# Performance work log

Measured on AMD Instinct MI355X. Metric: run time of the kernel, lower is better.

## Reference

```python
import jax, jax.numpy as jnp
import numpy as np

N_LIC, N_EMP, N_CON = 40000, 80000, 60000
D_LIC, D_EMP, D_CON = 256, 128, 192
H = 256
E_P, E_Q = 1280000, 640000


def setup_inputs() -> dict:
    key = jax.random.key(0)
    ks = jax.random.split(key, 13)
    s = 0.05
    return {
        "x_lic": jax.random.normal(ks[0], (N_LIC, D_LIC), jnp.float32),
        "x_emp": jax.random.normal(ks[1], (N_EMP, D_EMP), jnp.float32),
        "x_con": jax.random.normal(ks[2], (N_CON, D_CON), jnp.float32),
        "Wl_p": jax.random.normal(ks[3], (D_EMP, H), jnp.float32) * s,
        "Wr_p": jax.random.normal(ks[4], (D_LIC, H), jnp.float32) * s,
        "b_p": jax.random.normal(ks[5], (H,), jnp.float32) * s,
        "Wl_q": jax.random.normal(ks[6], (D_CON, H), jnp.float32) * s,
        "Wr_q": jax.random.normal(ks[7], (D_LIC, H), jnp.float32) * s,
        "b_q": jax.random.normal(ks[8], (H,), jnp.float32) * s,
        "ei_p_src": jax.random.randint(ks[9], (E_P,), 0, N_EMP, jnp.int64),
        "ei_p_dst": jax.random.randint(ks[10], (E_P,), 0, N_LIC, jnp.int64),
        "ei_q_src": jax.random.randint(ks[11], (E_Q,), 0, N_CON, jnp.int64),
        "ei_q_dst": jax.random.randint(ks[12], (E_Q,), 0, N_LIC, jnp.int64),
    }


def _sage_conv(x_src, x_dst, src, dst, Wl, Wr, b):
    """PyG SAGEConv (mean aggr): lin_l(mean_neighbors) + lin_r(x_dst) + bias."""
    n_dst = x_dst.shape[0]
    # gather src features per edge, scatter-sum to dst nodes
    agg = jax.ops.segment_sum(x_src[src], dst, num_segments=n_dst)  # [n_dst, d_src]
    deg = jax.ops.segment_sum(jnp.ones(src.shape, x_src.dtype), dst, num_segments=n_dst)
    agg = agg / jnp.maximum(deg, 1.0)[:, None]  # zero-degree nodes -> 0 (PyG semantics)
    return agg @ Wl + x_dst @ Wr + b


def reference(x_lic, x_emp, x_con, Wl_p, Wr_p, b_p, Wl_q, Wr_q, b_q,
              ei_p_src, ei_p_dst, ei_q_src, ei_q_dst):
    # to_hetero dispatch: two relations target 'licitacion'; aggr='mean' across relations.
    out_p = _sage_conv(x_emp, x_lic, ei_p_src, ei_p_dst, Wl_p, Wr_p, b_p)  # empresa->licitacion
    out_q = _sage_conv(x_con, x_lic, ei_q_src, ei_q_dst, Wl_q, Wr_q, b_q)  # contrato->licitacion
    # forward returns x_dict['licitacion'] after relu; other dst types are dead code.
    return jax.nn.relu(0.5 * (out_p + out_q))
```

## Files before the change

kernel.cpp:

```cpp
#include <hip/hip_runtime.h>

#define N_LIC 40000
#define N_EMP 80000
#define N_CON 60000
#define D_EMP 128
#define D_CON 192
#define HDIM  256
#define E_P   1280000
#define E_Q   640000
#define E_T   (E_P + E_Q)

#define NSEG  64
#define SEGW  (2 * NSEG)
#define SUBR  (N_LIC / NSEG)
#define NBPRE ((E_T + 2047) / 2048)

#define OFF_AGGP   0
#define OFF_STG    OFF_AGGP
#define OFF_XE     (OFF_AGGP + 2560000)
#define OFF_AGGQ   OFF_XE
#define OFF_XC     (OFF_XE + 5120000)
#define OFF_BPK    (OFF_XC + 5760000)
#define OFF_BIAS   (OFF_BPK + 73728)
#define OFF_CNT    (OFF_BIAS + 256)
#define OFF_SEGT   (OFF_CNT + 2 * N_LIC)
#define OFF_SEGB   (OFF_SEGT + 128)
#define OFF_SEGC   (OFF_SEGB + 128)
#define OFF_OFFP   (OFF_SEGC + 128)
#define OFF_OFFQ   (OFF_OFFP + N_LIC)
#define OFF_SRTP   (OFF_OFFQ + N_LIC)
#define OFF_SRTQ   (OFF_SRTP + E_P)

typedef short bf16x8 __attribute__((ext_vector_type(8)));
typedef float f32x4 __attribute__((ext_vector_type(4)));

__device__ __forceinline__ ushort f2bf(float f) {
    union { float f; uint u; } v; v.f = f;
    return (ushort)((v.u + 0x7fffu + ((v.u >> 16) & 1u)) >> 16);
}

__device__ __forceinline__ void acc2(uint u, float& lo, float& hi) {
    union { uint u; float f; } a, b;
    a.u = u << 16;
    b.u = u & 0xffff0000u;
    lo += a.f; hi += b.f;
}

__device__ __forceinline__ uint packbf(float lo, float hi) {
    return (uint)f2bf(lo) | ((uint)f2bf(hi) << 16);
}

__global__ void prep_kernel(const float* __restrict__ Wlp, const float* __restrict__ Wlq,
                            const float* __restrict__ Wrp, const float* __restrict__ Wrq,
                            const float* __restrict__ bp, const float* __restrict__ bq,
                            ushort* __restrict__ Bpk, float* __restrict__ bias) {
    int tid = blockIdx.x * 256 + threadIdx.x;
    if (tid < 256 * 576) {
        int n = tid / 576, k = tid - n * 576;
        float v;
        if (k < 128)      v = Wlp[k * 256 + n];
        else if (k < 320) v = Wlq[(k - 128) * 256 + n];
        else              v = Wrp[(k - 320) * 256 + n] + Wrq[(k - 320) * 256 + n];
        Bpk[tid] = f2bf(v);
    } else if (tid < 256 * 576 + 256) {
        int j = tid - 256 * 576;
        bias[j] = bp[j] + bq[j];
    }
}

#define C_XE (N_EMP * 128 / 4)
#define C_XC (N_CON * 192 / 4)
__global__ __launch_bounds__(256) void conv_pre_kernel(
        const float* __restrict__ xemp, const float* __restrict__ xcon,
        ushort* __restrict__ xe, ushort* __restrict__ xc,
        const int* __restrict__ dp, const int* __restrict__ dq,
        int* __restrict__ segtot) {
    __shared__ int lc[SEGW];
    int b = blockIdx.x;
    int t = threadIdx.x;
    if (b < NBPRE) {
        if (t < SEGW) lc[t] = 0;
        __syncthreads();
        int base = b * 2048 + t;
        #pragma unroll
        for (int i = 0; i < 8; i++) {
            int e = base + i * 256;
            if (e < E_T) {
                int d, rel;
                if (e < E_P) { d = __builtin_nontemporal_load(&dp[e]); rel = 0; }
                else         { d = __builtin_nontemporal_load(&dq[e - E_P]); rel = 1; }
                atomicAdd(&lc[rel * NSEG + d / SUBR], 1);
            }
        }
        __syncthreads();
        if (t < SEGW && lc[t] > 0) atomicAdd(&segtot[t], lc[t]);
    } else {
        int tid = (b - NBPRE) * 256 + t;
        const float* src; ushort* dst; int i;
        if (tid < C_XE) { src = xemp; dst = xe; i = tid; }
        else            { src = xcon; dst = xc; i = tid - C_XE; }
        float4 v = ((const float4*)src)[i];
        uint2 o;
        o.x = packbf(v.x, v.y);
        o.y = packbf(v.z, v.w);
        ((uint2*)dst)[i] = o;
    }
}

__global__ void segbase_kernel(const int* __restrict__ segtot,
                               int* __restrict__ segbase, int* __restrict__ segcur) {
    if (threadIdx.x == 0) {
        int run = 0;
        for (int i = 0; i < SEGW; i++) {
            segbase[i] = run; segcur[i] = run;
            run += segtot[i];
        }
    }
}

__global__ __launch_bounds__(256) void partition_kernel(const int* __restrict__ sp,
                                                        const int* __restrict__ dp,
                                                        const int* __restrict__ sq,
                                                        const int* __restrict__ dq,
                                                        int* __restrict__ segcur,
                                                        uint* __restrict__ stg) {
    __shared__ int lc[SEGW], inc[SEGW], lb[SEGW], gb[SEGW];
    __shared__ uint srtd[2048];
    __shared__ uchar sid[2048];
    int t = threadIdx.x;
    if (t < SEGW) lc[t] = 0;
    __syncthreads();
    int seg[8], lo[8]; uint pk[8];
    int base = blockIdx.x * 2048 + t;
    #pragma unroll
    for (int i = 0; i < 8; i++) {
        int e = base + i * 256;
        seg[i] = -1;
        if (e < E_T) {
            int d, s, rel;
            if (e < E_P) {
                d = __builtin_nontemporal_load(&dp[e]);
                s = __builtin_nontemporal_load(&sp[e]); rel = 0;
            } else {
                int eq = e - E_P;
                d = __builtin_nontemporal_load(&dq[eq]);
                s = __builtin_nontemporal_load(&sq[eq]); rel = 1;
            }
            int sl = d / SUBR;
            int dl = d - sl * SUBR;
            seg[i] = rel * NSEG + sl;
            pk[i] = ((uint)dl << 17) | (uint)s;
            lo[i] = atomicAdd(&lc[seg[i]], 1);
        }
    }
    __syncthreads();
    if (t < SEGW) inc[t] = lc[t];
    __syncthreads();
    #pragma unroll
    for (int off = 1; off < SEGW; off <<= 1) {
        int v = (t >= off && t < SEGW) ? inc[t - off] : 0;
        __syncthreads();
        if (t < SEGW) inc[t] += v;
        __syncthreads();
    }
    if (t < SEGW) {
        lb[t] = inc[t] - lc[t];
        gb[t] = lc[t] > 0 ? atomicAdd(&segcur[t], lc[t]) : 0;
    }
    __syncthreads();
    #pragma unroll
    for (int i = 0; i < 8; i++) {
        if (seg[i] >= 0) {
            int p = lb[seg[i]] + lo[i];
            srtd[p] = pk[i];
            sid[p] = (uchar)seg[i];
        }
    }
    __syncthreads();
    int tot = inc[SEGW - 1];
    for (int p = t; p < tot; p += 256) {
        int s = sid[p];
        stg[gb[s] + (p - lb[s])] = srtd[p];
    }
}

#define LCAP 22528
__global__ __launch_bounds__(1024) void sort_kernel(const int* __restrict__ segbase,
                                                    const int* __restrict__ segcur,
                                                    const uint* __restrict__ stg,
                                                    int* __restrict__ srtp, int* __restrict__ srtq,
                                                    int* __restrict__ offp, int* __restrict__ offq,
                                                    int* __restrict__ cnt) {
    __shared__ int lcnt[SUBR], lcur[SUBR];
    __shared__ int sc[640];
    __shared__ uint buf[LCAP];
    int s = blockIdx.x;
    int rel = s >> 6;
    int beg = segbase[s], end = segcur[s];
    int t = threadIdx.x;
    if (t < SUBR) { lcnt[t] = 0; lcur[t] = 0; }
    __syncthreads();
    for (int idx = beg + t; idx < end; idx += 1024)
        atomicAdd(&lcnt[stg[idx] >> 17], 1);
    __syncthreads();
    if (t < 640) sc[t] = (t < SUBR) ? lcnt[t] : 0;
    __syncthreads();
    #pragma unroll
    for (int off = 1; off < 640; off <<= 1) {
        int v = (t >= off && t < 640) ? sc[t - off] : 0;
        __syncthreads();
        if (t < 640) sc[t] += v;
        __syncthreads();
    }
    int rb = (rel == 0) ? beg : beg - E_P;
    int* srt = (rel == 0) ? srtp : srtq;
    for (int idx = beg + t; idx < end; idx += 1024) {
        uint p = stg[idx];
        int dl = (int)(p >> 17);
        int pos = sc[dl] - lcnt[dl] + atomicAdd(&lcur[dl], 1);
        uint sv = p & 0x1FFFFu;
        if (pos < LCAP) buf[pos] = sv;
        else srt[rb + pos] = (int)sv;
    }
    __syncthreads();
    int n = end - beg;
    int m = n < LCAP ? n : LCAP;
    for (int p = t; p < m; p += 1024) srt[rb + p] = (int)buf[p];
    int dbase = (s & (NSEG - 1)) * SUBR;
    int* offs = (rel == 0) ? offp : offq;
    int* cn = (rel == 0) ? cnt : cnt + N_LIC;
    if (t < SUBR) {
        offs[dbase + t] = rb + sc[t] - lcnt[t];
        cn[dbase + t] = lcnt[t];
    }
}

__global__ __launch_bounds__(256) void aggP_kernel(const ushort* __restrict__ xe,
                                                   const int* __restrict__ offs,
                                                   const int* __restrict__ cnt,
                                                   const int* __restrict__ sorted,
                                                   ushort* __restrict__ agg) {
    int g = blockIdx.x * 16 + (threadIdx.x >> 4);
    int c = threadIdx.x & 15;
    int beg = offs[g], deg = cnt[g], end = beg + deg;
    float a0=0,a1=0,a2=0,a3=0,a4=0,a5=0,a6=0,a7=0;
    int eb = beg;
    for (; eb + 16 <= end; eb += 16) {
        int my = sorted[eb + c];
        #pragma unroll
        for (int j = 0; j < 16; j++) {
            int s = __shfl(my, j, 16);
            uint4 v = *(const uint4*)(xe + (size_t)s * D_EMP + c * 8);
            acc2(v.x, a0, a1); acc2(v.y, a2, a3);
            acc2(v.z, a4, a5); acc2(v.w, a6, a7);
        }
    }
    int n = end - eb;
    if (n > 0) {
        int my = (c < n) ? sorted[eb + c] : 0;
        for (int j = 0; j < n; j++) {
            int s = __shfl(my, j, 16);
            uint4 v = *(const uint4*)(xe + (size_t)s * D_EMP + c * 8);
            acc2(v.x, a0, a1); acc2(v.y, a2, a3);
            acc2(v.z, a4, a5); acc2(v.w, a6, a7);
        }
    }
    float inv = 1.0f / fmaxf((float)deg, 1.0f);
    uint4 o;
    o.x = packbf(a0 * inv, a1 * inv);
    o.y = packbf(a2 * inv, a3 * inv);
    o.z = packbf(a4 * inv, a5 * inv);
    o.w = packbf(a6 * inv, a7 * inv);
    *(uint4*)(agg + (size_t)g * D_EMP + c * 8) = o;
}

__global__ __launch_bounds__(256) void aggQ_kernel(const ushort* __restrict__ xc,
                                                   const int* __restrict__ offs,
                                                   const int* __restrict__ cnt,
                                                   const int* __restrict__ sorted,
                                                   ushort* __restrict__ agg) {
    int g = blockIdx.x * 16 + (threadIdx.x >> 4);
    int c = threadIdx.x & 15;
    int beg = offs[g], deg = cnt[g], end = beg + deg;
    float a0=0,a1=0,a2=0,a3=0,a4=0,a5=0,a6=0,a7=0,a8=0,a9=0,a10=0,a11=0;
    int eb = beg;
    for (; eb + 16 <= end; eb += 16) {
        int my = sorted[eb + c];
        #pragma unroll 8
        for (int j = 0; j < 16; j++) {
            int s = __shfl(my, j, 16);
            const ushort* row = xc + (size_t)s * D_CON + c * 12;
            uint2 v0 = *(const uint2*)(row + 0);
            uint2 v1 = *(const uint2*)(row + 4);
            uint2 v2 = *(const uint2*)(row + 8);
            acc2(v0.x, a0, a1);  acc2(v0.y, a2, a3);
            acc2(v1.x, a4, a5);  acc2(v1.y, a6, a7);
            acc2(v2.x, a8, a9);  acc2(v2.y, a10, a11);
        }
    }
    int n = end - eb;
    if (n > 0) {
        int my = (c < n) ? sorted[eb + c] : 0;
        for (int j = 0; j < n; j++) {
            int s = __shfl(my, j, 16);
            const ushort* row = xc + (size_t)s * D_CON + c * 12;
            uint2 v0 = *(const uint2*)(row + 0);
            uint2 v1 = *(const uint2*)(row + 4);
            uint2 v2 = *(const uint2*)(row + 8);
            acc2(v0.x, a0, a1);  acc2(v0.y, a2, a3);
            acc2(v1.x, a4, a5);  acc2(v1.y, a6, a7);
            acc2(v2.x, a8, a9);  acc2(v2.y, a10, a11);
        }
    }
    float inv = 1.0f / fmaxf((float)deg, 1.0f);
    ushort* o = agg + (size_t)g * D_CON + c * 12;
    uint2 w0, w1, w2;
    w0.x = packbf(a0 * inv, a1 * inv);   w0.y = packbf(a2 * inv, a3 * inv);
    w1.x = packbf(a4 * inv, a5 * inv);   w1.y = packbf(a6 * inv, a7 * inv);
    w2.x = packbf(a8 * inv, a9 * inv);   w2.y = packbf(a10 * inv, a11 * inv);
    *(uint2*)(o + 0) = w0;
    *(uint2*)(o + 4) = w1;
    *(uint2*)(o + 8) = w2;
}

__global__ __launch_bounds__(256) void gemm_kernel(
    const ushort* __restrict__ aggp, const ushort* __restrict__ aggq,
    const float* __restrict__ xlic, const ushort* __restrict__ Bpk,
    const float* __restrict__ bias, float* __restrict__ out)
{
    __shared__ __align__(16) ushort As[2][64 * 40];
    __shared__ __align__(16) ushort Bs[2][256 * 40];

    const int t = threadIdx.x;
    const int m0 = blockIdx.x * 64;
    const int lane = t & 63;
    const int wave = t >> 6;
    const int arow = t >> 2;
    const int achk = t & 3;
    const int l15 = lane & 15;
    const int lh  = lane >> 4;

    f32x4 acc[4][4];
    #pragma unroll
    for (int i = 0; i < 4; i++)
        #pragma unroll
        for (int j = 0; j < 4; j++)
            acc[i][j] = (f32x4){0.f, 0.f, 0.f, 0.f};

    uint4 pb0, pb1, pb2, pb3, pa0, pa1;

    #define REG_LOAD(k0)                                                                     \
    {                                                                                        \
        pb0 = *(const uint4*)(Bpk + (size_t)(arow +   0) * 576 + (k0) + achk * 8);           \
        pb1 = *(const uint4*)(Bpk + (size_t)(arow +  64) * 576 + (k0) + achk * 8);           \
        pb2 = *(const uint4*)(Bpk + (size_t)(arow + 128) * 576 + (k0) + achk * 8);           \
        pb3 = *(const uint4*)(Bpk + (size_t)(arow + 192) * 576 + (k0) + achk * 8);           \
        if ((k0) < 128) {                                                                    \
            pa0 = *(const uint4*)(aggp + (size_t)(m0 + arow) * 128 + (k0) + achk * 8);       \
        } else if ((k0) < 320) {                                                             \
            pa0 = *(const uint4*)(aggq + (size_t)(m0 + arow) * 192 + ((k0) - 128) + achk * 8); \
        } else {                                                                             \
            const float* src_ = xlic + (size_t)(m0 + arow) * 256 + ((k0) - 320) + achk * 8;  \
            pa0 = *(const uint4*)(src_ + 0);                                                 \
            pa1 = *(const uint4*)(src_ + 4);                                                 \
        }                                                                                    \
    }

    #define LDS_WRITE(b, k0)                                                                 \
    {                                                                                        \
        uint4 aw;                                                                            \
        if ((k0) < 320) aw = pa0;                                                            \
        else {                                                                               \
            union { uint4 u; float f[4]; } c0, c1;                                           \
            c0.u = pa0; c1.u = pa1;                                                          \
            aw.x = packbf(c0.f[0], c0.f[1]);                                                 \
            aw.y = packbf(c0.f[2], c0.f[3]);                                                 \
            aw.z = packbf(c1.f[0], c1.f[1]);                                                 \
            aw.w = packbf(c1.f[2], c1.f[3]);                                                 \
        }                                                                                    \
        *(uint4*)(&As[b][arow * 40 + achk * 8]) = aw;                                        \
        *(uint4*)(&Bs[b][(arow +   0) * 40 + achk * 8]) = pb0;                               \
        *(uint4*)(&Bs[b][(arow +  64) * 40 + achk * 8]) = pb1;                               \
        *(uint4*)(&Bs[b][(arow + 128) * 40 + achk * 8]) = pb2;                               \
        *(uint4*)(&Bs[b][(arow + 192) * 40 + achk * 8]) = pb3;                               \
    }

    #define COMPUTE(b)                                                                       \
    {                                                                                        \
        bf16x8 af[4], bfr[4];                                                                \
        _Pragma("unroll")                                                                    \
        for (int mt = 0; mt < 4; mt++)                                                       \
            af[mt] = *(const bf16x8*)(&As[b][(mt * 16 + l15) * 40 + lh * 8]);                \
        _Pragma("unroll")                                                                    \
        for (int nt = 0; nt < 4; nt++)                                                       \
            bfr[nt] = *(const bf16x8*)(&Bs[b][(wave * 64 + nt * 16 + l15) * 40 + lh * 8]);   \
        _Pragma("unroll")                                                                    \
        for (int mt = 0; mt < 4; mt++)                                                       \
            _Pragma("unroll")                                                                \
            for (int nt = 0; nt < 4; nt++)                                                   \
                acc[mt][nt] = __builtin_amdgcn_mfma_f32_16x16x32_bf16(af[mt], bfr[nt], acc[mt][nt], 0, 0, 0); \
    }

    REG_LOAD(0);
    LDS_WRITE(0, 0);
    __syncthreads();

    int cur = 0;
    for (int k0 = 32; k0 < 576; k0 += 32) {
        REG_LOAD(k0);
        COMPUTE(cur);
        LDS_WRITE(cur ^ 1, k0);
        __syncthreads();
        cur ^= 1;
    }
    COMPUTE(cur);

    #pragma unroll
    for (int nt = 0; nt < 4; nt++) {
        int n = wave * 64 + nt * 16 + l15;
        float bv = bias[n];
        #pragma unroll
        for (int mt = 0; mt < 4; mt++) {
            #pragma unroll
            for (int r = 0; r < 4; r++) {
                int m = m0 + mt * 16 + lh * 4 + r;
                float v = 0.5f * (acc[mt][nt][r] + bv);
                out[(size_t)m * 256 + n] = fmaxf(v, 0.f);
            }
        }
    }
    #undef REG_LOAD
    #undef LDS_WRITE
    #undef COMPUTE
}

extern "C" void kernel_launch(void* const* d_in, const int* in_sizes, int n_in,
                              void* d_out, int out_size, void* d_ws, size_t ws_size,
                              hipStream_t stream) {
    const float* x_lic = (const float*)d_in[0];
    const float* x_emp = (const float*)d_in[1];
    const float* x_con = (const float*)d_in[2];
    const float* Wl_p  = (const float*)d_in[3];
    const float* Wr_p  = (const float*)d_in[4];
    const float* b_p   = (const float*)d_in[5];
    const float* Wl_q  = (const float*)d_in[6];
    const float* Wr_q  = (const float*)d_in[7];
    const float* b_q   = (const float*)d_in[8];
    const int* ei_p_src = (const int*)d_in[9];
    const int* ei_p_dst = (const int*)d_in[10];
    const int* ei_q_src = (const int*)d_in[11];
    const int* ei_q_dst = (const int*)d_in[12];

    float* ws = (float*)d_ws;
    ushort* aggp = (ushort*)(ws + OFF_AGGP);
    ushort* aggq = (ushort*)(ws + OFF_AGGQ);
    uint*  stg  = (uint*)(ws + OFF_STG);
    ushort* xe   = (ushort*)(ws + OFF_XE);
    ushort* xc   = (ushort*)(ws + OFF_XC);
    ushort* Bpk  = (ushort*)(ws + OFF_BPK);
    float* bias  = ws + OFF_BIAS;
    int* cnt  = (int*)(ws + OFF_CNT);
    int* segt = (int*)(ws + OFF_SEGT);
    int* segb = (int*)(ws + OFF_SEGB);
    int* segc = (int*)(ws + OFF_SEGC);
    int* offp = (int*)(ws + OFF_OFFP);
    int* offq = (int*)(ws + OFF_OFFQ);
    int* srtp = (int*)(ws + OFF_SRTP);
    int* srtq = (int*)(ws + OFF_SRTQ);
    float* out = (float*)d_out;

    hipMemsetAsync(segt, 0, SEGW * sizeof(int), stream);

    prep_kernel<<<(256 * 576 + 256 + 255) / 256, 256, 0, stream>>>(Wl_p, Wl_q, Wr_p, Wr_q, b_p, b_q, Bpk, bias);

    conv_pre_kernel<<<NBPRE + (C_XE + C_XC) / 256, 256, 0, stream>>>(
        x_emp, x_con, xe, xc, ei_p_dst, ei_q_dst, segt);

    segbase_kernel<<<1, 64, 0, stream>>>(segt, segb, segc);
    partition_kernel<<<NBPRE, 256, 0, stream>>>(ei_p_src, ei_p_dst, ei_q_src, ei_q_dst, segc, stg);

    sort_kernel<<<SEGW, 1024, 0, stream>>>(segb, segc, stg, srtp, srtq, offp, offq, cnt);

    aggP_kernel<<<N_LIC / 16, 256, 0, stream>>>(xe, offp, cnt, srtp, aggp);
    aggQ_kernel<<<N_LIC / 16, 256, 0, stream>>>(xc, offq, cnt + N_LIC, srtq, aggq);

    gemm_kernel<<<N_LIC / 64, 256, 0, stream>>>(aggp, aggq, x_lic, Bpk, bias, out);
}
```

Before: 354.6 us.

## Fuse neighbor aggregation for both relations into the GEMM kernel

```diff
diff --git a/kernel.cpp b/kernel.cpp
--- a/kernel.cpp
+++ b/kernel.cpp
@@ -18,7 +18,6 @@
 #define OFF_AGGP   0
 #define OFF_STG    OFF_AGGP
 #define OFF_XE     (OFF_AGGP + 2560000)
-#define OFF_AGGQ   OFF_XE
 #define OFF_XC     (OFF_XE + 5120000)
 #define OFF_BPK    (OFF_XC + 5760000)
 #define OFF_BIAS   (OFF_BPK + 73728)
@@ -235,104 +234,105 @@
     }
 }
 
-__global__ __launch_bounds__(256) void aggP_kernel(const ushort* __restrict__ xe,
-                                                   const int* __restrict__ offs,
-                                                   const int* __restrict__ cnt,
-                                                   const int* __restrict__ sorted,
-                                                   ushort* __restrict__ agg) {
-    int g = blockIdx.x * 16 + (threadIdx.x >> 4);
-    int c = threadIdx.x & 15;
-    int beg = offs[g], deg = cnt[g], end = beg + deg;
-    float a0=0,a1=0,a2=0,a3=0,a4=0,a5=0,a6=0,a7=0;
-    int eb = beg;
-    for (; eb + 16 <= end; eb += 16) {
-        int my = sorted[eb + c];
-        #pragma unroll
-        for (int j = 0; j < 16; j++) {
-            int s = __shfl(my, j, 16);
-            uint4 v = *(const uint4*)(xe + (size_t)s * D_EMP + c * 8);
-            acc2(v.x, a0, a1); acc2(v.y, a2, a3);
-            acc2(v.z, a4, a5); acc2(v.w, a6, a7);
-        }
-    }
-    int n = end - eb;
-    if (n > 0) {
-        int my = (c < n) ? sorted[eb + c] : 0;
-        for (int j = 0; j < n; j++) {
-            int s = __shfl(my, j, 16);
-            uint4 v = *(const uint4*)(xe + (size_t)s * D_EMP + c * 8);
-            acc2(v.x, a0, a1); acc2(v.y, a2, a3);
-            acc2(v.z, a4, a5); acc2(v.w, a6, a7);
-        }
-    }
-    float inv = 1.0f / fmaxf((float)deg, 1.0f);
-    uint4 o;
-    o.x = packbf(a0 * inv, a1 * inv);
-    o.y = packbf(a2 * inv, a3 * inv);
-    o.z = packbf(a4 * inv, a5 * inv);
-    o.w = packbf(a6 * inv, a7 * inv);
-    *(uint4*)(agg + (size_t)g * D_EMP + c * 8) = o;
-}
-
-__global__ __launch_bounds__(256) void aggQ_kernel(const ushort* __restrict__ xc,
-                                                   const int* __restrict__ offs,
-                                                   const int* __restrict__ cnt,
-                                                   const int* __restrict__ sorted,
-                                                   ushort* __restrict__ agg) {
-    int g = blockIdx.x * 16 + (threadIdx.x >> 4);
-    int c = threadIdx.x & 15;
-    int beg = offs[g], deg = cnt[g], end = beg + deg;
-    float a0=0,a1=0,a2=0,a3=0,a4=0,a5=0,a6=0,a7=0,a8=0,a9=0,a10=0,a11=0;
-    int eb = beg;
-    for (; eb + 16 <= end; eb += 16) {
-        int my = sorted[eb + c];
-        #pragma unroll 8
-        for (int j = 0; j < 16; j++) {
-            int s = __shfl(my, j, 16);
-            const ushort* row = xc + (size_t)s * D_CON + c * 12;
-            uint2 v0 = *(const uint2*)(row + 0);
-            uint2 v1 = *(const uint2*)(row + 4);
-            uint2 v2 = *(const uint2*)(row + 8);
-            acc2(v0.x, a0, a1);  acc2(v0.y, a2, a3);
-            acc2(v1.x, a4, a5);  acc2(v1.y, a6, a7);
-            acc2(v2.x, a8, a9);  acc2(v2.y, a10, a11);
-        }
-    }
-    int n = end - eb;
-    if (n > 0) {
-        int my = (c < n) ? sorted[eb + c] : 0;
-        for (int j = 0; j < n; j++) {
-            int s = __shfl(my, j, 16);
-            const ushort* row = xc + (size_t)s * D_CON + c * 12;
-            uint2 v0 = *(const uint2*)(row + 0);
-            uint2 v1 = *(const uint2*)(row + 4);
-            uint2 v2 = *(const uint2*)(row + 8);
-            acc2(v0.x, a0, a1);  acc2(v0.y, a2, a3);
-            acc2(v1.x, a4, a5);  acc2(v1.y, a6, a7);
-            acc2(v2.x, a8, a9);  acc2(v2.y, a10, a11);
-        }
-    }
-    float inv = 1.0f / fmaxf((float)deg, 1.0f);
-    ushort* o = agg + (size_t)g * D_CON + c * 12;
-    uint2 w0, w1, w2;
-    w0.x = packbf(a0 * inv, a1 * inv);   w0.y = packbf(a2 * inv, a3 * inv);
-    w1.x = packbf(a4 * inv, a5 * inv);   w1.y = packbf(a6 * inv, a7 * inv);
-    w2.x = packbf(a8 * inv, a9 * inv);   w2.y = packbf(a10 * inv, a11 * inv);
-    *(uint2*)(o + 0) = w0;
-    *(uint2*)(o + 4) = w1;
-    *(uint2*)(o + 8) = w2;
-}
-
-__global__ __launch_bounds__(256) void gemm_kernel(
-    const ushort* __restrict__ aggp, const ushort* __restrict__ aggq,
-    const float* __restrict__ xlic, const ushort* __restrict__ Bpk,
-    const float* __restrict__ bias, float* __restrict__ out)
+#define AQP 200
+__global__ __launch_bounds__(256) void fused_kernel(
+        const ushort* __restrict__ xe, const ushort* __restrict__ xc,
+        const int* __restrict__ offp, const int* __restrict__ offq,
+        const int* __restrict__ cnt,
+        const int* __restrict__ srtp, const int* __restrict__ srtq,
+        const float* __restrict__ xlic, const ushort* __restrict__ Bpk,
+        const float* __restrict__ bias,
+        ushort* __restrict__ aggp, float* __restrict__ out)
 {
-    __shared__ __align__(16) ushort As[2][64 * 40];
+    __shared__ __align__(16) ushort Aq[64 * AQP];
     __shared__ __align__(16) ushort Bs[2][256 * 40];
 
     const int t = threadIdx.x;
     const int m0 = blockIdx.x * 64;
+
+    {
+        int nd = t >> 4, c = t & 15;
+        for (int r = 0; r < 4; r++) {
+            int g = m0 + r * 16 + nd;
+            int beg = offp[g], deg = cnt[g], end = beg + deg;
+            float a0=0,a1=0,a2=0,a3=0,a4=0,a5=0,a6=0,a7=0;
+            int eb = beg;
+            for (; eb + 16 <= end; eb += 16) {
+                int my = srtp[eb + c];
+                #pragma unroll
+                for (int j = 0; j < 16; j++) {
+                    int s = __shfl(my, j, 16);
+                    uint4 v = *(const uint4*)(xe + (size_t)s * D_EMP + c * 8);
+                    acc2(v.x, a0, a1); acc2(v.y, a2, a3);
+                    acc2(v.z, a4, a5); acc2(v.w, a6, a7);
+                }
+            }
+            int n = end - eb;
+            if (n > 0) {
+                int my = (c < n) ? srtp[eb + c] : 0;
+                for (int j = 0; j < n; j++) {
+                    int s = __shfl(my, j, 16);
+                    uint4 v = *(const uint4*)(xe + (size_t)s * D_EMP + c * 8);
+                    acc2(v.x, a0, a1); acc2(v.y, a2, a3);
+                    acc2(v.z, a4, a5); acc2(v.w, a6, a7);
+                }
+            }
+            float inv = 1.0f / fmaxf((float)deg, 1.0f);
+            uint4 o;
+            o.x = packbf(a0 * inv, a1 * inv);
+            o.y = packbf(a2 * inv, a3 * inv);
+            o.z = packbf(a4 * inv, a5 * inv);
+            o.w = packbf(a6 * inv, a7 * inv);
+            *(uint4*)(aggp + (size_t)g * D_EMP + c * 8) = o;
+        }
+
+        for (int r = 0; r < 4; r++) {
+            int lrow = r * 16 + nd;
+            int g = m0 + lrow;
+            int beg = offq[g], deg = cnt[N_LIC + g], end = beg + deg;
+            float a0=0,a1=0,a2=0,a3=0,a4=0,a5=0,a6=0,a7=0,a8=0,a9=0,a10=0,a11=0;
+            int eb = beg;
+            for (; eb + 16 <= end; eb += 16) {
+                int my = srtq[eb + c];
+                #pragma unroll 8
+                for (int j = 0; j < 16; j++) {
+                    int s = __shfl(my, j, 16);
+                    const ushort* row = xc + (size_t)s * D_CON + c * 12;
+                    uint2 v0 = *(const uint2*)(row + 0);
+                    uint2 v1 = *(const uint2*)(row + 4);
+                    uint2 v2 = *(const uint2*)(row + 8);
+                    acc2(v0.x, a0, a1);  acc2(v0.y, a2, a3);
+                    acc2(v1.x, a4, a5);  acc2(v1.y, a6, a7);
+                    acc2(v2.x, a8, a9);  acc2(v2.y, a10, a11);
+                }
+            }
+            int n = end - eb;
+            if (n > 0) {
+                int my = (c < n) ? srtq[eb + c] : 0;
+                for (int j = 0; j < n; j++) {
+                    int s = __shfl(my, j, 16);
+                    const ushort* row = xc + (size_t)s * D_CON + c * 12;
+                    uint2 v0 = *(const uint2*)(row + 0);
+                    uint2 v1 = *(const uint2*)(row + 4);
+                    uint2 v2 = *(const uint2*)(row + 8);
+                    acc2(v0.x, a0, a1);  acc2(v0.y, a2, a3);
+                    acc2(v1.x, a4, a5);  acc2(v1.y, a6, a7);
+                    acc2(v2.x, a8, a9);  acc2(v2.y, a10, a11);
+                }
+            }
+            float inv = 1.0f / fmaxf((float)deg, 1.0f);
+            ushort* o = Aq + lrow * AQP + c * 12;
+            uint2 w0, w1, w2;
+            w0.x = packbf(a0 * inv, a1 * inv);   w0.y = packbf(a2 * inv, a3 * inv);
+            w1.x = packbf(a4 * inv, a5 * inv);   w1.y = packbf(a6 * inv, a7 * inv);
+            w2.x = packbf(a8 * inv, a9 * inv);   w2.y = packbf(a10 * inv, a11 * inv);
+            *(uint2*)(o + 0) = w0;
+            *(uint2*)(o + 4) = w1;
+            *(uint2*)(o + 8) = w2;
+        }
+    }
+    __syncthreads();
+
     const int lane = t & 63;
     const int wave = t >> 6;
     const int arow = t >> 2;
@@ -347,73 +347,71 @@
         for (int j = 0; j < 4; j++)
             acc[i][j] = (f32x4){0.f, 0.f, 0.f, 0.f};
 
-    uint4 pb0, pb1, pb2, pb3, pa0, pa1;
-
-    #define REG_LOAD(k0)                                                                     \
+    uint4 pb0, pb1, pb2, pb3;
+
+    #define REG_LOAD_B(k0)                                                                   \
     {                                                                                        \
         pb0 = *(const uint4*)(Bpk + (size_t)(arow +   0) * 576 + (k0) + achk * 8);           \
         pb1 = *(const uint4*)(Bpk + (size_t)(arow +  64) * 576 + (k0) + achk * 8);           \
         pb2 = *(const uint4*)(Bpk + (size_t)(arow + 128) * 576 + (k0) + achk * 8);           \
         pb3 = *(const uint4*)(Bpk + (size_t)(arow + 192) * 576 + (k0) + achk * 8);           \
-        if ((k0) < 128) {                                                                    \
-            pa0 = *(const uint4*)(aggp + (size_t)(m0 + arow) * 128 + (k0) + achk * 8);       \
-        } else if ((k0) < 320) {                                                             \
-            pa0 = *(const uint4*)(aggq + (size_t)(m0 + arow) * 192 + ((k0) - 128) + achk * 8); \
-        } else {                                                                             \
-            const float* src_ = xlic + (size_t)(m0 + arow) * 256 + ((k0) - 320) + achk * 8;  \
-            pa0 = *(const uint4*)(src_ + 0);                                                 \
-            pa1 = *(const uint4*)(src_ + 4);                                                 \
-        }                                                                                    \
-    }
-
-    #define LDS_WRITE(b, k0)                                                                 \
+    }
+    #define LDS_WRITE_B(b)                                                                   \
     {                                                                                        \
-        uint4 aw;                                                                            \
-        if ((k0) < 320) aw = pa0;                                                            \
-        else {                                                                               \
-            union { uint4 u; float f[4]; } c0, c1;                                           \
-            c0.u = pa0; c1.u = pa1;                                                          \
-            aw.x = packbf(c0.f[0], c0.f[1]);                                                 \
-            aw.y = packbf(c0.f[2], c0.f[3]);                                                 \
-            aw.z = packbf(c1.f[0], c1.f[1]);                                                 \
-            aw.w = packbf(c1.f[2], c1.f[3]);                                                 \
-        }                                                                                    \
-        *(uint4*)(&As[b][arow * 40 + achk * 8]) = aw;                                        \
         *(uint4*)(&Bs[b][(arow +   0) * 40 + achk * 8]) = pb0;                               \
         *(uint4*)(&Bs[b][(arow +  64) * 40 + achk * 8]) = pb1;                               \
         *(uint4*)(&Bs[b][(arow + 128) * 40 + achk * 8]) = pb2;                               \
         *(uint4*)(&Bs[b][(arow + 192) * 40 + achk * 8]) = pb3;                               \
     }
 
-    #define COMPUTE(b)                                                                       \
-    {                                                                                        \
-        bf16x8 af[4], bfr[4];                                                                \
-        _Pragma("unroll")                                                                    \
-        for (int mt = 0; mt < 4; mt++)                                                       \
-            af[mt] = *(const bf16x8*)(&As[b][(mt * 16 + l15) * 40 + lh * 8]);                \
-        _Pragma("unroll")                                                                    \
-        for (int nt = 0; nt < 4; nt++)                                                       \
-            bfr[nt] = *(const bf16x8*)(&Bs[b][(wave * 64 + nt * 16 + l15) * 40 + lh * 8]);   \
-        _Pragma("unroll")                                                                    \
-        for (int mt = 0; mt < 4; mt++)                                                       \
-            _Pragma("unroll")                                                                \
-            for (int nt = 0; nt < 4; nt++)                                                   \
-                acc[mt][nt] = __builtin_amdgcn_mfma_f32_16x16x32_bf16(af[mt], bfr[nt], acc[mt][nt], 0, 0, 0); \
-    }
-
-    REG_LOAD(0);
-    LDS_WRITE(0, 0);
+    REG_LOAD_B(0);
+    LDS_WRITE_B(0);
     __syncthreads();
 
     int cur = 0;
-    for (int k0 = 32; k0 < 576; k0 += 32) {
-        REG_LOAD(k0);
-        COMPUTE(cur);
-        LDS_WRITE(cur ^ 1, k0);
-        __syncthreads();
-        cur ^= 1;
-    }
-    COMPUTE(cur);
+    for (int k0 = 32; k0 <= 576; k0 += 32) {
+        const int kk = k0 - 32;
+        bf16x8 af[4];
+        if (kk < 128) {
+            #pragma unroll
+            for (int mt = 0; mt < 4; mt++)
+                af[mt] = *(const bf16x8*)(aggp + (size_t)(m0 + mt * 16 + l15) * 128 + kk + lh * 8);
+        } else if (kk < 320) {
+            #pragma unroll
+            for (int mt = 0; mt < 4; mt++)
+                af[mt] = *(const bf16x8*)(&Aq[(mt * 16 + l15) * AQP + (kk - 128) + lh * 8]);
+        } else {
+            #pragma unroll
+            for (int mt = 0; mt < 4; mt++) {
+                const float* src = xlic + (size_t)(m0 + mt * 16 + l15) * 256 + (kk - 320) + lh * 8;
+                float4 v0 = *(const float4*)(src + 0);
+                float4 v1 = *(const float4*)(src + 4);
+                union { uint4 u; bf16x8 b; } cv;
+                cv.u.x = packbf(v0.x, v0.y);
+                cv.u.y = packbf(v0.z, v0.w);
+                cv.u.z = packbf(v1.x, v1.y);
+                cv.u.w = packbf(v1.z, v1.w);
+                af[mt] = cv.b;
+            }
+        }
+        if (k0 < 576) REG_LOAD_B(k0);
+
+        bf16x8 bfr[4];
+        #pragma unroll
+        for (int nt = 0; nt < 4; nt++)
+            bfr[nt] = *(const bf16x8*)(&Bs[cur][(wave * 64 + nt * 16 + l15) * 40 + lh * 8]);
+        #pragma unroll
+        for (int mt = 0; mt < 4; mt++)
+            #pragma unroll
+            for (int nt = 0; nt < 4; nt++)
+                acc[mt][nt] = __builtin_amdgcn_mfma_f32_16x16x32_bf16(af[mt], bfr[nt], acc[mt][nt], 0, 0, 0);
+
+        if (k0 < 576) {
+            LDS_WRITE_B(cur ^ 1);
+            __syncthreads();
+            cur ^= 1;
+        }
+    }
 
     #pragma unroll
     for (int nt = 0; nt < 4; nt++) {
@@ -429,9 +427,8 @@
             }
         }
     }
-    #undef REG_LOAD
-    #undef LDS_WRITE
-    #undef COMPUTE
+    #undef REG_LOAD_B
+    #undef LDS_WRITE_B
 }
 
 extern "C" void kernel_launch(void* const* d_in, const int* in_sizes, int n_in,
@@ -453,7 +450,6 @@
 
     float* ws = (float*)d_ws;
     ushort* aggp = (ushort*)(ws + OFF_AGGP);
-    ushort* aggq = (ushort*)(ws + OFF_AGGQ);
     uint*  stg  = (uint*)(ws + OFF_STG);
     ushort* xe   = (ushort*)(ws + OFF_XE);
     ushort* xc   = (ushort*)(ws + OFF_XC);
@@ -481,8 +477,6 @@
 
     sort_kernel<<<SEGW, 1024, 0, stream>>>(segb, segc, stg, srtp, srtq, offp, offq, cnt);
 
-    aggP_kernel<<<N_LIC / 16, 256, 0, stream>>>(xe, offp, cnt, srtp, aggp);
-    aggQ_kernel<<<N_LIC / 16, 256, 0, stream>>>(xc, offq, cnt + N_LIC, srtq, aggq);
-
-    gemm_kernel<<<N_LIC / 64, 256, 0, stream>>>(aggp, aggq, x_lic, Bpk, bias, out);
-}
+    fused_kernel<<<N_LIC / 64, 256, 0, stream>>>(xe, xc, offp, offq, cnt, srtp, srtq,
+                                                 x_lic, Bpk, bias, aggp, out);
+}
```

New measurement: 413.3 us. 16.5% more time.
